# Optimization experiments

Hardware: AMD Instinct MI355X
Metric: run time of the kernel (lower is better)

## Reference

```python
import jax, jax.numpy as jnp
import numpy as np

NEG = -1000000000.0
TEMP = 0.5
K = 15
EPS = 1e-5


def _bn(x, g, b):
    # BatchNorm1d in training mode: batch mean, biased variance
    mu = jnp.mean(x, axis=0)
    var = jnp.mean((x - mu) ** 2, axis=0)
    return (x - mu) * jax.lax.rsqrt(var + EPS) * g + b


def _lrelu(x):
    return jnp.where(x > 0, x, 0.2 * x)


def setup_inputs() -> dict:
    key = jax.random.key(0)
    ks = jax.random.split(key, 8)
    B, L = 131072, 50
    inp = {
        "z": jax.random.normal(ks[0], (B, L), jnp.float32),
        "u": jax.random.uniform(ks[1], (K, B, 25), jnp.float32),
        "W1": jax.random.normal(ks[2], (L, 128), jnp.float32) * 0.1,
        "b1": jnp.zeros((128,), jnp.float32),
        "g1": jnp.ones((128,), jnp.float32),
        "be1": jnp.zeros((128,), jnp.float32),
        "W2": jax.random.normal(ks[3], (128, 256), jnp.float32) * 0.1,
        "b2": jnp.zeros((256,), jnp.float32),
        "g2": jnp.ones((256,), jnp.float32),
        "be2": jnp.zeros((256,), jnp.float32),
        "W3": jax.random.normal(ks[4], (256, 128), jnp.float32) * 0.1,
        "b3": jnp.zeros((128,), jnp.float32),
        "g3": jnp.ones((128,), jnp.float32),
        "be3": jnp.zeros((128,), jnp.float32),
        "W4": jax.random.normal(ks[5], (128, 25), jnp.float32) * 0.1,
        "b4": jnp.zeros((25,), jnp.float32),
    }
    return inp


def reference(z, u, W1, b1, g1, be1, W2, b2, g2, be2, W3, b3, g3, be3, W4, b4):
    h = _lrelu(_bn(z @ W1 + b1, g1, be1))
    h = _lrelu(_bn(h @ W2 + b2, g2, be2))
    h = _lrelu(_bn(h @ W3 + b3, g3, be3))
    logits = h @ W4 + b4  # [B, 25]

    def step(mask, u_i):
        masked = jnp.where(mask, logits, NEG)
        noise = -jnp.log(-jnp.log(u_i))
        gumbel = (masked + noise) / TEMP
        probs = jax.nn.softmax(gumbel, axis=-1)
        idx = jnp.argmax(probs, axis=-1)  # [B]
        onehot = jax.nn.one_hot(idx, 25, dtype=bool)
        return mask & ~onehot, idx

    mask0 = jnp.ones(logits.shape, dtype=bool)
    _, idxs = jax.lax.scan(step, mask0, u)  # idxs: [K, B]
    selected = idxs.T.astype(jnp.float32) + 1.0  # [B, K], selected_idx + 1
    return (selected - 1.0) / 24.0
```

## Files before the change

kernel.cpp:

```cpp
#include <hip/hip_runtime.h>
#include <math.h>

#define BATCH 131072

template<int MT, int NT, int NSTORE, int TM, int TN, int BLK, bool AFFINE, bool STATS>
__global__ __launch_bounds__(BLK, 2)
void gemm_bn(const float* __restrict__ Ain, int K,
             const float* __restrict__ W, const float* __restrict__ bias,
             const float* __restrict__ sc, const float* __restrict__ sh,
             float* __restrict__ Xout,
             double* __restrict__ gsum, double* __restrict__ gsq)
{
    constexpr int KS  = 32;
    constexpr int MP  = MT + 4;
    constexpr int NP  = NT + 4;
    constexpr int NCG = NT / TN;
    constexpr int RG  = MT / TM;
    constexpr int NH  = TN / 4;
    static_assert(BLK == NCG * RG, "thread mapping");
    static_assert(!STATS || 2 * RG * NP <= KS * NP, "stats reuse of Bs");

    __shared__ float As[KS][MP];
    __shared__ float Bs[KS][NP];

    const int tid = threadIdx.x;
    const int r0  = blockIdx.x * MT;
    const int tx  = tid % NCG;
    const int ty  = tid / NCG;

    float acc[TM][TN] = {};

    const int KC = (K + KS - 1) / KS;
    for (int kc = 0; kc < KC; ++kc) {
        const int kbase = kc * KS;
        __syncthreads();
        constexpr int AL = MT * KS / BLK;
        #pragma unroll
        for (int l = 0; l < AL; ++l) {
            int idx = tid + l * BLK;
            int i = idx >> 5;
            int j = idx & 31;
            int gk = kbase + j;
            float v;
            if (AFFINE) {
                v = Ain[(size_t)(r0 + i) * K + gk];
                v = v * sc[gk] + sh[gk];
                v = v > 0.f ? v : 0.2f * v;
            } else {
                v = (gk < K) ? Ain[(size_t)(r0 + i) * K + gk] : 0.f;
            }
            As[j][i] = v;
        }
        constexpr int BL = NT * KS / BLK;
        #pragma unroll
        for (int l = 0; l < BL; ++l) {
            int idx = tid + l * BLK;
            int kk = idx / NT;
            int n  = idx % NT;
            int gk = kbase + kk;
            float v = 0.f;
            if (gk < K && n < NSTORE) v = W[(size_t)gk * NSTORE + n];
            Bs[kk][n] = v;
        }
        __syncthreads();
        #pragma unroll 2
        for (int k = 0; k < KS; ++k) {
            float a[TM], b[TN];
            #pragma unroll
            for (int i4 = 0; i4 < TM; i4 += 4)
                *reinterpret_cast<float4*>(&a[i4]) =
                    *reinterpret_cast<const float4*>(&As[k][ty * TM + i4]);
            #pragma unroll
            for (int h = 0; h < NH; ++h)
                *reinterpret_cast<float4*>(&b[h * 4]) =
                    *reinterpret_cast<const float4*>(&Bs[k][h * (NCG * 4) + tx * 4]);
            #pragma unroll
            for (int i = 0; i < TM; ++i)
                #pragma unroll
                for (int j = 0; j < TN; ++j)
                    acc[i][j] = fmaf(a[i], b[j], acc[i][j]);
        }
    }

    float bc[TN];
    #pragma unroll
    for (int j = 0; j < TN; ++j) {
        int gc = (j >> 2) * (NCG * 4) + tx * 4 + (j & 3);
        bc[j] = (gc < NSTORE) ? bias[gc] : 0.f;
    }
    float psum[TN] = {};
    float psq[TN]  = {};
    #pragma unroll
    for (int i = 0; i < TM; ++i) {
        int row = r0 + ty * TM + i;
        float x[TN];
        #pragma unroll
        for (int j = 0; j < TN; ++j) {
            x[j] = acc[i][j] + bc[j];
            psum[j] += x[j];
            psq[j]  += x[j] * x[j];
        }
        if (NSTORE == NT) {
            #pragma unroll
            for (int h = 0; h < NH; ++h) {
                float4 v = make_float4(x[h*4], x[h*4+1], x[h*4+2], x[h*4+3]);
                *reinterpret_cast<float4*>(
                    &Xout[(size_t)row * NSTORE + h * (NCG * 4) + tx * 4]) = v;
            }
        } else {
            #pragma unroll
            for (int j = 0; j < TN; ++j) {
                int gc = (j >> 2) * (NCG * 4) + tx * 4 + (j & 3);
                if (gc < NSTORE) Xout[(size_t)row * NSTORE + gc] = x[j];
            }
        }
    }

    if (STATS) {
        __syncthreads();
        float* S1 = &Bs[0][0];
        float* S2 = S1 + RG * NP;
        #pragma unroll
        for (int j = 0; j < TN; ++j) {
            int gc = (j >> 2) * (NCG * 4) + tx * 4 + (j & 3);
            S1[ty * NP + gc] = psum[j];
            S2[ty * NP + gc] = psq[j];
        }
        __syncthreads();
        if (tid < NT) {
            double s = 0.0, q = 0.0;
            #pragma unroll 4
            for (int t = 0; t < RG; ++t) {
                s += (double)S1[t * NP + tid];
                q += (double)S2[t * NP + tid];
            }
            atomicAdd(&gsum[tid], s);
            atomicAdd(&gsq[tid], q);
        }
    }
}

__global__ void finalize_bn(const double* __restrict__ sum, const double* __restrict__ sq,
                            const float* __restrict__ g, const float* __restrict__ be,
                            float* __restrict__ sc, float* __restrict__ sh, int N)
{
    int i = threadIdx.x;
    if (i < N) {
        const double inv = 1.0 / (double)BATCH;
        double mu  = sum[i] * inv;
        double var = sq[i] * inv - mu * mu;
        double s   = (double)g[i] / sqrt(var + 1e-5);
        sc[i] = (float)s;
        sh[i] = (float)((double)be[i] - mu * s);
    }
}

__global__ __launch_bounds__(256)
void gumbel_topk(const float* __restrict__ logits, const float* __restrict__ u,
                 float* __restrict__ out)
{
    __shared__ float lg[256 * 25];
    __shared__ float us[256 * 25];
    const int tid = threadIdx.x;
    const int r0  = blockIdx.x * 256;

    for (int idx = tid; idx < 256 * 25; idx += 256)
        lg[idx] = logits[(size_t)r0 * 25 + idx];
    __syncthreads();

    float myl[25];
    #pragma unroll
    for (int j = 0; j < 25; ++j) myl[j] = lg[tid * 25 + j];

    unsigned mask = 0x1FFFFFFu;
    for (int it = 0; it < 15; ++it) {
        __syncthreads();
        const float* uk = u + ((size_t)it * BATCH + r0) * 25;
        for (int idx = tid; idx < 256 * 25; idx += 256)
            us[idx] = uk[idx];
        __syncthreads();

        float best = -INFINITY;
        int bj = 0;
        #pragma unroll
        for (int j = 0; j < 25; ++j) {
            float uu = us[tid * 25 + j];
            float nz = -logf(-logf(uu));
            float v  = myl[j] + nz;
            v = ((mask >> j) & 1u) ? v : -INFINITY;
            if (v > best) { best = v; bj = j; }
        }
        mask &= ~(1u << bj);
        out[(size_t)(r0 + tid) * 15 + it] = (float)bj / 24.0f;
    }
}

extern "C" void kernel_launch(void* const* d_in, const int* in_sizes, int n_in,
                              void* d_out, int out_size, void* d_ws, size_t ws_size,
                              hipStream_t stream)
{
    (void)in_sizes; (void)n_in; (void)out_size; (void)ws_size;
    const float* z   = (const float*)d_in[0];
    const float* u   = (const float*)d_in[1];
    const float* W1  = (const float*)d_in[2];
    const float* b1  = (const float*)d_in[3];
    const float* g1  = (const float*)d_in[4];
    const float* be1 = (const float*)d_in[5];
    const float* W2  = (const float*)d_in[6];
    const float* b2  = (const float*)d_in[7];
    const float* g2  = (const float*)d_in[8];
    const float* be2 = (const float*)d_in[9];
    const float* W3  = (const float*)d_in[10];
    const float* b3  = (const float*)d_in[11];
    const float* g3  = (const float*)d_in[12];
    const float* be3 = (const float*)d_in[13];
    const float* W4  = (const float*)d_in[14];
    const float* b4  = (const float*)d_in[15];
    float* out = (float*)d_out;

    char* ws = (char*)d_ws;
    float* X2     = (float*)ws;
    float* XA     = (float*)(ws + (size_t)134217728);
    char*  statb  = ws + (size_t)134217728 + (size_t)67108864;
    double* sum1 = (double*)statb;      double* sq1 = sum1 + 128;
    double* sum2 = sq1 + 128;           double* sq2 = sum2 + 256;
    double* sum3 = sq2 + 256;           double* sq3 = sum3 + 128;
    float* sc1 = (float*)(sq3 + 128);   float* sh1 = sc1 + 128;
    float* sc2 = sh1 + 128;             float* sh2 = sc2 + 256;
    float* sc3 = sh2 + 256;             float* sh3 = sc3 + 128;
    float* logits = X2;

    hipMemsetAsync(statb, 0, 1024 * sizeof(double), stream);

    gemm_bn<256,128,128, 16,8, 256, false, true>
        <<<BATCH/256, 256, 0, stream>>>(z, 50, W1, b1, nullptr, nullptr, XA, sum1, sq1);
    finalize_bn<<<1, 256, 0, stream>>>(sum1, sq1, g1, be1, sc1, sh1, 128);

    gemm_bn<128,256,256, 16,8, 256, true, true>
        <<<BATCH/128, 256, 0, stream>>>(XA, 128, W2, b2, sc1, sh1, X2, sum2, sq2);
    finalize_bn<<<1, 256, 0, stream>>>(sum2, sq2, g2, be2, sc2, sh2, 256);

    gemm_bn<256,128,128, 16,8, 256, true, true>
        <<<BATCH/256, 256, 0, stream>>>(X2, 256, W3, b3, sc2, sh2, XA, sum3, sq3);
    finalize_bn<<<1, 256, 0, stream>>>(sum3, sq3, g3, be3, sc3, sh3, 128);

    gemm_bn<256,32,25, 8,4, 256, true, false>
        <<<BATCH/256, 256, 0, stream>>>(XA, 128, W4, b4, sc3, sh3, logits, nullptr, nullptr);

    gumbel_topk<<<BATCH/256, 256, 0, stream>>>(logits, u, out);
}
```

Before: 871.1 us.

## Double-buffer GEMM staging with register prefetch, row-major swizzled A tiles, vector loads

Restructures the fused GEMM+BN kernel so that global loads for the next K-chunk go into registers while the current chunk is computed, with double-buffered shared tiles. A is stored row-major in shared memory with an XOR swizzle and loaded as float4. The BN scale and shift vectors are cached in shared memory, and the first layer uses a single 64-wide K chunk. Tile sizes also shrink (smaller MT, TM) to raise block count, and gumbel_topk copies into shared memory with float4 loads. The trade-offs are higher register and shared-memory pressure and more template complexity.

```diff
diff --git a/kernel.cpp b/kernel.cpp
--- a/kernel.cpp
+++ b/kernel.cpp
@@ -3,82 +3,224 @@
 
 #define BATCH 131072
 
-template<int MT, int NT, int NSTORE, int TM, int TN, int BLK, bool AFFINE, bool STATS>
-__global__ __launch_bounds__(BLK, 2)
-void gemm_bn(const float* __restrict__ Ain, int K,
-             const float* __restrict__ W, const float* __restrict__ bias,
-             const float* __restrict__ sc, const float* __restrict__ sh,
-             float* __restrict__ Xout,
+template<int MT, int NT, int NSTORE, int TM, int TN, int BLK, int KS, int KPAD,
+         int KRT, bool AFFINE, bool STATS>
+__global__ __launch_bounds__(BLK)
+void gemm_bn(const float* __restrict__ Ain, const float* __restrict__ W,
+             const float* __restrict__ bias, const float* __restrict__ sc,
+             const float* __restrict__ sh, float* __restrict__ Xout,
              double* __restrict__ gsum, double* __restrict__ gsq)
 {
-    constexpr int KS  = 32;
-    constexpr int MP  = MT + 4;
-    constexpr int NP  = NT + 4;
+    constexpr int KC  = KPAD / KS;
+    constexpr int DB  = (KC > 1) ? 2 : 1;
+    constexpr int CPR = KS / 4;
     constexpr int NCG = NT / TN;
     constexpr int RG  = MT / TM;
     constexpr int NH  = TN / 4;
-    static_assert(BLK == NCG * RG, "thread mapping");
-    static_assert(!STATS || 2 * RG * NP <= KS * NP, "stats reuse of Bs");
-
-    __shared__ float As[KS][MP];
-    __shared__ float Bs[KS][NP];
+    constexpr int AL4 = MT * KS / 4 / BLK;
+    constexpr bool BVEC = (NT == NSTORE);
+    constexpr int BL4 = BVEC ? (KS * NT / 4 / BLK) : 1;
+    constexpr int BLS = BVEC ? 1 : (KS * NT / BLK);
+    static_assert(NCG * RG == BLK, "thread mapping");
+    static_assert(MT * KS >= 4 * BLK, "A staging divisibility");
+    static_assert(!STATS || 2 * RG * NT <= DB * KS * NT, "stats scratch fits Bs");
+
+    __shared__ float As[DB][MT][KS];
+    __shared__ float Bs[DB][KS][NT];
+    __shared__ float scs[AFFINE ? KPAD : 1];
+    __shared__ float shs[AFFINE ? KPAD : 1];
 
     const int tid = threadIdx.x;
     const int r0  = blockIdx.x * MT;
     const int tx  = tid % NCG;
     const int ty  = tid / NCG;
+    const int sty = ty & 3;
 
     float acc[TM][TN] = {};
 
-    const int KC = (K + KS - 1) / KS;
-    for (int kc = 0; kc < KC; ++kc) {
-        const int kbase = kc * KS;
-        __syncthreads();
-        constexpr int AL = MT * KS / BLK;
-        #pragma unroll
-        for (int l = 0; l < AL; ++l) {
+    auto loadA = [&](int kc, float4* av) {
+        #pragma unroll
+        for (int l = 0; l < AL4; ++l) {
             int idx = tid + l * BLK;
-            int i = idx >> 5;
-            int j = idx & 31;
-            int gk = kbase + j;
-            float v;
-            if (AFFINE) {
-                v = Ain[(size_t)(r0 + i) * K + gk];
-                v = v * sc[gk] + sh[gk];
-                v = v > 0.f ? v : 0.2f * v;
+            int row = idx / CPR;
+            int c4  = idx % CPR;
+            int gk  = kc * KS + c4 * 4;
+            const float* gp = Ain + (size_t)(r0 + row) * KRT + gk;
+            if constexpr (KRT == KPAD) {
+                av[l] = *reinterpret_cast<const float4*>(gp);
             } else {
-                v = (gk < K) ? Ain[(size_t)(r0 + i) * K + gk] : 0.f;
-            }
-            As[j][i] = v;
-        }
-        constexpr int BL = NT * KS / BLK;
-        #pragma unroll
-        for (int l = 0; l < BL; ++l) {
+                if (gk + 4 <= KRT) av[l] = *reinterpret_cast<const float4*>(gp);
+                else {
+                    float t[4];
+                    #pragma unroll
+                    for (int c = 0; c < 4; ++c) t[c] = (gk + c < KRT) ? gp[c] : 0.f;
+                    av[l] = make_float4(t[0], t[1], t[2], t[3]);
+                }
+            }
+        }
+    };
+    auto storeA = [&](int kc, const float4* av, int d) {
+        #pragma unroll
+        for (int l = 0; l < AL4; ++l) {
             int idx = tid + l * BLK;
-            int kk = idx / NT;
-            int n  = idx % NT;
-            int gk = kbase + kk;
-            float v = 0.f;
-            if (gk < K && n < NSTORE) v = W[(size_t)gk * NSTORE + n];
-            Bs[kk][n] = v;
-        }
+            int row = idx / CPR;
+            int c4  = idx % CPR;
+            float4 v = av[l];
+            if constexpr (AFFINE) {
+                int k0 = kc * KS + c4 * 4;
+                float* vp = &v.x;
+                #pragma unroll
+                for (int c = 0; c < 4; ++c) {
+                    float x = vp[c] * scs[k0 + c] + shs[k0 + c];
+                    vp[c] = x > 0.f ? x : 0.2f * x;
+                }
+            }
+            int p = c4 ^ ((row / TM) & 3);
+            *reinterpret_cast<float4*>(&As[d][row][p * 4]) = v;
+        }
+    };
+    auto loadB = [&](int kc, float4* bv, float* bsc) {
+        if constexpr (BVEC) {
+            #pragma unroll
+            for (int l = 0; l < BL4; ++l) {
+                int idx = tid + l * BLK;
+                int kk  = idx / (NT / 4);
+                int n4  = idx % (NT / 4);
+                int gk  = kc * KS + kk;
+                if constexpr (KRT == KPAD)
+                    bv[l] = *reinterpret_cast<const float4*>(W + (size_t)gk * NSTORE + n4 * 4);
+                else
+                    bv[l] = (gk < KRT)
+                        ? *reinterpret_cast<const float4*>(W + (size_t)gk * NSTORE + n4 * 4)
+                        : make_float4(0.f, 0.f, 0.f, 0.f);
+            }
+        } else {
+            #pragma unroll
+            for (int l = 0; l < BLS; ++l) {
+                int idx = tid + l * BLK;
+                int kk  = idx / NT;
+                int n   = idx % NT;
+                int gk  = kc * KS + kk;
+                bsc[l] = (gk < KRT && n < NSTORE) ? W[(size_t)gk * NSTORE + n] : 0.f;
+            }
+        }
+    };
+    auto storeB = [&](const float4* bv, const float* bsc, int d) {
+        if constexpr (BVEC) {
+            #pragma unroll
+            for (int l = 0; l < BL4; ++l) {
+                int idx = tid + l * BLK;
+                int kk  = idx / (NT / 4);
+                int n4  = idx % (NT / 4);
+                *reinterpret_cast<float4*>(&Bs[d][kk][n4 * 4]) = bv[l];
+            }
+        } else {
+            #pragma unroll
+            for (int l = 0; l < BLS; ++l) {
+                int idx = tid + l * BLK;
+                Bs[d][idx / NT][idx % NT] = bsc[l];
+            }
+        }
+    };
+    auto compute = [&](int d) {
+        #pragma unroll
+        for (int k4 = 0; k4 < CPR; ++k4) {
+            float4 a4[TM];
+            const int p = (k4 ^ sty);
+            #pragma unroll
+            for (int i = 0; i < TM; ++i)
+                a4[i] = *reinterpret_cast<const float4*>(&As[d][ty * TM + i][p * 4]);
+            #pragma unroll
+            for (int kk = 0; kk < 4; ++kk) {
+                float b[TN];
+                #pragma unroll
+                for (int h = 0; h < NH; ++h)
+                    *reinterpret_cast<float4*>(&b[h * 4]) =
+                        *reinterpret_cast<const float4*>(&Bs[d][k4 * 4 + kk][h * (NCG * 4) + tx * 4]);
+                #pragma unroll
+                for (int i = 0; i < TM; ++i) {
+                    const float av = (&a4[i].x)[kk];
+                    #pragma unroll
+                    for (int j = 0; j < TN; ++j)
+                        acc[i][j] = fmaf(av, b[j], acc[i][j]);
+                }
+            }
+        }
+    };
+
+    if constexpr (AFFINE) {
+        if (tid < KPAD) { scs[tid] = sc[tid]; shs[tid] = sh[tid]; }
+    }
+
+    if constexpr (KC == 1) {
+        if constexpr (AFFINE) __syncthreads();
+        #pragma unroll
+        for (int l0 = 0; l0 < AL4; l0 += 4) {
+            float4 t[4];
+            constexpr int NB = (AL4 < 4) ? AL4 : 4;
+            #pragma unroll
+            for (int q = 0; q < NB; ++q) {
+                float4 tv[1];
+                int idx = tid + (l0 + q) * BLK;
+                int row = idx / CPR;
+                int c4  = idx % CPR;
+                int gk  = c4 * 4;
+                const float* gp = Ain + (size_t)(r0 + row) * KRT + gk;
+                if (gk + 4 <= KRT) tv[0] = *reinterpret_cast<const float4*>(gp);
+                else {
+                    float tt[4];
+                    #pragma unroll
+                    for (int c = 0; c < 4; ++c) tt[c] = (gk + c < KRT) ? gp[c] : 0.f;
+                    tv[0] = make_float4(tt[0], tt[1], tt[2], tt[3]);
+                }
+                t[q] = tv[0];
+            }
+            #pragma unroll
+            for (int q = 0; q < NB; ++q) {
+                int idx = tid + (l0 + q) * BLK;
+                int row = idx / CPR;
+                int c4  = idx % CPR;
+                int p   = c4 ^ ((row / TM) & 3);
+                *reinterpret_cast<float4*>(&As[0][row][p * 4]) = t[q];
+            }
+        }
+        #pragma unroll
+        for (int l0 = 0; l0 < BL4; l0 += 4) {
+            float4 t[4];
+            constexpr int NB = (BL4 < 4) ? BL4 : 4;
+            #pragma unroll
+            for (int q = 0; q < NB; ++q) {
+                int idx = tid + (l0 + q) * BLK;
+                int kk  = idx / (NT / 4);
+                int n4  = idx % (NT / 4);
+                t[q] = (kk < KRT)
+                    ? *reinterpret_cast<const float4*>(W + (size_t)kk * NSTORE + n4 * 4)
+                    : make_float4(0.f, 0.f, 0.f, 0.f);
+            }
+            #pragma unroll
+            for (int q = 0; q < NB; ++q) {
+                int idx = tid + (l0 + q) * BLK;
+                *reinterpret_cast<float4*>(&Bs[0][idx / (NT / 4)][(idx % (NT / 4)) * 4]) = t[q];
+            }
+        }
+        __syncthreads();
+        compute(0);
+        __syncthreads();
+    } else {
+        float4 av[AL4];
+        float4 bv[BL4];
+        float  bsc[BLS];
+        loadA(0, av); loadB(0, bv, bsc);
+        if constexpr (AFFINE) __syncthreads();
+        storeA(0, av, 0); storeB(bv, bsc, 0);
         __syncthreads();
         #pragma unroll 2
-        for (int k = 0; k < KS; ++k) {
-            float a[TM], b[TN];
-            #pragma unroll
-            for (int i4 = 0; i4 < TM; i4 += 4)
-                *reinterpret_cast<float4*>(&a[i4]) =
-                    *reinterpret_cast<const float4*>(&As[k][ty * TM + i4]);
-            #pragma unroll
-            for (int h = 0; h < NH; ++h)
-                *reinterpret_cast<float4*>(&b[h * 4]) =
-                    *reinterpret_cast<const float4*>(&Bs[k][h * (NCG * 4) + tx * 4]);
-            #pragma unroll
-            for (int i = 0; i < TM; ++i)
-                #pragma unroll
-                for (int j = 0; j < TN; ++j)
-                    acc[i][j] = fmaf(a[i], b[j], acc[i][j]);
+        for (int kc = 0; kc < KC; ++kc) {
+            const int cur = kc & 1;
+            if (kc + 1 < KC) { loadA(kc + 1, av); loadB(kc + 1, bv, bsc); }
+            compute(cur);
+            if (kc + 1 < KC) { storeA(kc + 1, av, cur ^ 1); storeB(bv, bsc, cur ^ 1); }
+            __syncthreads();
         }
     }
 
@@ -88,8 +230,7 @@
         int gc = (j >> 2) * (NCG * 4) + tx * 4 + (j & 3);
         bc[j] = (gc < NSTORE) ? bias[gc] : 0.f;
     }
-    float psum[TN] = {};
-    float psq[TN]  = {};
+    float psum[TN] = {}, psq[TN] = {};
     #pragma unroll
     for (int i = 0; i < TM; ++i) {
         int row = r0 + ty * TM + i;
@@ -97,10 +238,9 @@
         #pragma unroll
         for (int j = 0; j < TN; ++j) {
             x[j] = acc[i][j] + bc[j];
-            psum[j] += x[j];
-            psq[j]  += x[j] * x[j];
-        }
-        if (NSTORE == NT) {
+            if (STATS) { psum[j] += x[j]; psq[j] += x[j] * x[j]; }
+        }
+        if constexpr (BVEC) {
             #pragma unroll
             for (int h = 0; h < NH; ++h) {
                 float4 v = make_float4(x[h*4], x[h*4+1], x[h*4+2], x[h*4+3]);
@@ -115,24 +255,22 @@
             }
         }
     }
-
-    if (STATS) {
-        __syncthreads();
-        float* S1 = &Bs[0][0];
-        float* S2 = S1 + RG * NP;
+    if constexpr (STATS) {
+        float* S1 = &Bs[0][0][0];
+        float* S2 = S1 + RG * NT;
         #pragma unroll
         for (int j = 0; j < TN; ++j) {
             int gc = (j >> 2) * (NCG * 4) + tx * 4 + (j & 3);
-            S1[ty * NP + gc] = psum[j];
-            S2[ty * NP + gc] = psq[j];
+            S1[ty * NT + gc] = psum[j];
+            S2[ty * NT + gc] = psq[j];
         }
         __syncthreads();
         if (tid < NT) {
             double s = 0.0, q = 0.0;
             #pragma unroll 4
             for (int t = 0; t < RG; ++t) {
-                s += (double)S1[t * NP + tid];
-                q += (double)S2[t * NP + tid];
+                s += (double)S1[t * NT + tid];
+                q += (double)S2[t * NT + tid];
             }
             atomicAdd(&gsum[tid], s);
             atomicAdd(&gsq[tid], q);
@@ -159,13 +297,16 @@
 void gumbel_topk(const float* __restrict__ logits, const float* __restrict__ u,
                  float* __restrict__ out)
 {
-    __shared__ float lg[256 * 25];
-    __shared__ float us[256 * 25];
+    __shared__ __align__(16) float lg[256 * 25];
+    __shared__ __align__(16) float us[256 * 25];
     const int tid = threadIdx.x;
     const int r0  = blockIdx.x * 256;
 
-    for (int idx = tid; idx < 256 * 25; idx += 256)
-        lg[idx] = logits[(size_t)r0 * 25 + idx];
+    {
+        const float4* src = reinterpret_cast<const float4*>(logits + (size_t)r0 * 25);
+        float4* dst = reinterpret_cast<float4*>(lg);
+        for (int i = tid; i < 1600; i += 256) dst[i] = src[i];
+    }
     __syncthreads();
 
     float myl[25];
@@ -175,9 +316,9 @@
     unsigned mask = 0x1FFFFFFu;
     for (int it = 0; it < 15; ++it) {
         __syncthreads();
-        const float* uk = u + ((size_t)it * BATCH + r0) * 25;
-        for (int idx = tid; idx < 256 * 25; idx += 256)
-            us[idx] = uk[idx];
+        const float4* usrc = reinterpret_cast<const float4*>(u + ((size_t)it * BATCH + r0) * 25);
+        float4* ud = reinterpret_cast<float4*>(us);
+        for (int i = tid; i < 1600; i += 256) ud[i] = usrc[i];
         __syncthreads();
 
         float best = -INFINITY;
@@ -232,20 +373,20 @@
 
     hipMemsetAsync(statb, 0, 1024 * sizeof(double), stream);
 
-    gemm_bn<256,128,128, 16,8, 256, false, true>
-        <<<BATCH/256, 256, 0, stream>>>(z, 50, W1, b1, nullptr, nullptr, XA, sum1, sq1);
+    gemm_bn<128,128,128, 8,8, 256, 64, 64, 50, false, true>
+        <<<BATCH/128, 256, 0, stream>>>(z, W1, b1, nullptr, nullptr, XA, sum1, sq1);
     finalize_bn<<<1, 256, 0, stream>>>(sum1, sq1, g1, be1, sc1, sh1, 128);
 
-    gemm_bn<128,256,256, 16,8, 256, true, true>
-        <<<BATCH/128, 256, 0, stream>>>(XA, 128, W2, b2, sc1, sh1, X2, sum2, sq2);
+    gemm_bn<64,256,256, 8,8, 256, 16, 128, 128, true, true>
+        <<<BATCH/64, 256, 0, stream>>>(XA, W2, b2, sc1, sh1, X2, sum2, sq2);
     finalize_bn<<<1, 256, 0, stream>>>(sum2, sq2, g2, be2, sc2, sh2, 256);
 
-    gemm_bn<256,128,128, 16,8, 256, true, true>
-        <<<BATCH/256, 256, 0, stream>>>(X2, 256, W3, b3, sc2, sh2, XA, sum3, sq3);
+    gemm_bn<128,128,128, 8,8, 256, 16, 256, 256, true, true>
+        <<<BATCH/128, 256, 0, stream>>>(X2, W3, b3, sc2, sh2, XA, sum3, sq3);
     finalize_bn<<<1, 256, 0, stream>>>(sum3, sq3, g3, be3, sc3, sh3, 128);
 
-    gemm_bn<256,32,25, 8,4, 256, true, false>
-        <<<BATCH/256, 256, 0, stream>>>(XA, 128, W4, b4, sc3, sh3, logits, nullptr, nullptr);
+    gemm_bn<128,32,25, 4,4, 256, 16, 128, 128, true, false>
+        <<<BATCH/128, 256, 0, stream>>>(XA, W4, b4, sc3, sh3, logits, nullptr, nullptr);
 
     gumbel_topk<<<BATCH/256, 256, 0, stream>>>(logits, u, out);
 }
```

Result: slower. 1.357 ms (+55.8%).
